# Kernel tuning notes

Measured on AMD Instinct MI355X. Metric: run time of the kernel, lower is better.

Reference implementation:

```python
import jax, jax.numpy as jnp
import numpy as np

GAMMA = 0.99
LMBDA = 0.95


def setup_inputs() -> dict:
    key = jax.random.key(0)
    k1, k2, k3, k4 = jax.random.split(key, 4)
    B, T = 8192, 2048
    reward = jax.random.normal(k1, (B, T), dtype=jnp.float32)
    terminated = jax.random.randint(k2, (B, T), 0, 2).astype(jnp.bool_)
    value = jax.random.normal(k3, (B, T), dtype=jnp.float32)
    next_value = jax.random.normal(k4, (B, T), dtype=jnp.float32)
    return {"reward": reward, "terminated": terminated, "value": value, "next_value": next_value}


def reference(reward, terminated, value, next_value):
    # not_done: [B, T]
    not_done = 1.0 - terminated.astype(reward.dtype)
    # fake_bootstrap=False branch: zero out next_value at terminal steps
    delta = reward + GAMMA * (next_value * not_done) - value  # [B, T]
    coef = (GAMMA * LMBDA) * not_done                          # [B, T]

    def step(gae, xs):
        d_t, c_t = xs                 # each [B]
        gae = d_t + c_t * gae
        return gae, gae

    init = jnp.zeros(reward.shape[0], dtype=reward.dtype)
    # scan backward in time over [T, B] slices; reverse=True keeps outputs
    # aligned with the original time indices.
    _, adv_t = jax.lax.scan(step, init, (delta.T, coef.T), reverse=True)
    advantages = adv_t.T              # [B, T]
    returns = advantages + value
    return advantages, returns
```

## Files before the change

### kernel.cpp

```cpp
#include <hip/hip_runtime.h>


#define GAMMA 0.99f
#define LMBDA 0.95f

constexpr int T_LEN      = 2048;
constexpr int PER_THREAD = 4;
constexpr int BLOCK      = T_LEN / PER_THREAD;
constexpr int NWAVE      = BLOCK / 64;

__global__ __launch_bounds__(BLOCK) void gae_kernel(
    const float* __restrict__ reward,
    const int*   __restrict__ terminated,
    const float* __restrict__ value,
    const float* __restrict__ next_value,
    float* __restrict__ adv_out,
    float* __restrict__ ret_out)
{
    const int b   = blockIdx.x;
    const int j   = threadIdx.x;
    const size_t base = (size_t)b * T_LEN + (size_t)j * PER_THREAD;

    float4 r0 = *(const float4*)(reward     + base);
    float4 v0 = *(const float4*)(value      + base);
    float4 n0 = *(const float4*)(next_value + base);
    int4   tA = *(const int4*)  (terminated + base);

    float rr[4] = {r0.x, r0.y, r0.z, r0.w};
    float vv[4] = {v0.x, v0.y, v0.z, v0.w};
    float nn[4] = {n0.x, n0.y, n0.z, n0.w};
    int   tt[4] = {tA.x, tA.y, tA.z, tA.w};

    float delta[4], coef[4];
#pragma unroll
    for (int i = 0; i < 4; ++i) {
        float nd = tt[i] ? 0.0f : 1.0f;
        delta[i] = rr[i] + GAMMA * nn[i] * nd - vv[i];
        coef[i]  = (GAMMA * LMBDA) * nd;
    }

    float A = 0.0f, P = 1.0f;
#pragma unroll
    for (int i = 3; i >= 0; --i) {
        A = delta[i] + coef[i] * A;
        P = coef[i] * P;
    }

    const int lane = j & 63;
    const int wave = j >> 6;
    float SA = A, SP = P;
#pragma unroll
    for (int o = 1; o < 64; o <<= 1) {
        float A2 = __shfl_down(SA, o, 64);
        float P2 = __shfl_down(SP, o, 64);
        if (lane + o < 64) {
            SA = SA + SP * A2;
            SP = SP * P2;
        }
    }
    float EA = __shfl_down(SA, 1, 64);
    float EP = __shfl_down(SP, 1, 64);
    if (lane == 63) { EA = 0.0f; EP = 1.0f; }

    __shared__ float wA[NWAVE];
    __shared__ float wP[NWAVE];
    if (lane == 0) { wA[wave] = SA; wP[wave] = SP; }
    __syncthreads();

    float accA = 0.0f;
    for (int ww = NWAVE - 1; ww > wave; --ww) {
        accA = wA[ww] + wP[ww] * accA;
    }

    float g = EA + EP * accA;

    float adv[4];
#pragma unroll
    for (int i = 3; i >= 0; --i) {
        g = delta[i] + coef[i] * g;
        adv[i] = g;
    }

    float4 a0 = {adv[0], adv[1], adv[2], adv[3]};
    float4 q0 = {adv[0] + vv[0], adv[1] + vv[1], adv[2] + vv[2], adv[3] + vv[3]};

    *(float4*)(adv_out + base) = a0;
    *(float4*)(ret_out + base) = q0;
}

extern "C" void kernel_launch(void* const* d_in, const int* in_sizes, int n_in,
                              void* d_out, int out_size, void* d_ws, size_t ws_size,
                              hipStream_t stream) {
    const float* reward     = (const float*)d_in[0];
    const int*   terminated = (const int*)  d_in[1];
    const float* value      = (const float*)d_in[2];
    const float* next_value = (const float*)d_in[3];

    const int total = in_sizes[0];
    const int B     = total / T_LEN;

    float* adv = (float*)d_out;
    float* ret = (float*)d_out + (size_t)total;

    gae_kernel<<<B, BLOCK, 0, stream>>>(reward, terminated, value, next_value, adv, ret);
}
```

Measured before the change: 317.0 us.

## Process each row with a single wave over eight segments, dropping LDS sync

Replaces the 512-thread block per row, which needed a cross-wave shared-memory combine and __syncthreads, with one 64-lane wave per row. Each lane handles 8 segments of 4 elements, and the segment carries are combined through wave shuffles plus a short serial chain over lane-0 values. This removes the block barrier and LDS traffic and gives more independent shuffle chains to interleave. In exchange it uses many more registers per thread (about 32 loaded floats per input array), which may lower occupancy in a memory-bound kernel, and each wave has more serial work.

Result: no change. 321.8 us (+1.5%).

```diff
diff --git a/kernel.cpp b/kernel.cpp
--- a/kernel.cpp
+++ b/kernel.cpp
@@ -4,12 +4,11 @@
 #define GAMMA 0.99f
 #define LMBDA 0.95f
 
-constexpr int T_LEN      = 2048;
-constexpr int PER_THREAD = 4;
-constexpr int BLOCK      = T_LEN / PER_THREAD;
-constexpr int NWAVE      = BLOCK / 64;
+constexpr int T_LEN  = 2048;
+constexpr int SEGS   = 8;
+constexpr int SEGLEN = 256;
 
-__global__ __launch_bounds__(BLOCK) void gae_kernel(
+__global__ __launch_bounds__(64) void gae_kernel(
     const float* __restrict__ reward,
     const int*   __restrict__ terminated,
     const float* __restrict__ value,
@@ -17,75 +16,94 @@
     float* __restrict__ adv_out,
     float* __restrict__ ret_out)
 {
-    const int b   = blockIdx.x;
-    const int j   = threadIdx.x;
-    const size_t base = (size_t)b * T_LEN + (size_t)j * PER_THREAD;
+    const int b    = blockIdx.x;
+    const int lane = threadIdx.x;
+    const size_t rowbase = (size_t)b * T_LEN;
 
-    float4 r0 = *(const float4*)(reward     + base);
-    float4 v0 = *(const float4*)(value      + base);
-    float4 n0 = *(const float4*)(next_value + base);
-    int4   tA = *(const int4*)  (terminated + base);
-
-    float rr[4] = {r0.x, r0.y, r0.z, r0.w};
-    float vv[4] = {v0.x, v0.y, v0.z, v0.w};
-    float nn[4] = {n0.x, n0.y, n0.z, n0.w};
-    int   tt[4] = {tA.x, tA.y, tA.z, tA.w};
-
-    float delta[4], coef[4];
+    float4 R[SEGS], V[SEGS], N[SEGS];
+    int4   Tm[SEGS];
 #pragma unroll
-    for (int i = 0; i < 4; ++i) {
-        float nd = tt[i] ? 0.0f : 1.0f;
-        delta[i] = rr[i] + GAMMA * nn[i] * nd - vv[i];
-        coef[i]  = (GAMMA * LMBDA) * nd;
+    for (int i = 0; i < SEGS; ++i) {
+        const size_t off = rowbase + (size_t)i * SEGLEN + (size_t)lane * 4;
+        R[i]  = *(const float4*)(reward     + off);
+        V[i]  = *(const float4*)(value      + off);
+        N[i]  = *(const float4*)(next_value + off);
+        Tm[i] = *(const int4*)  (terminated + off);
     }
 
-    float A = 0.0f, P = 1.0f;
+    float delta[SEGS][4], coef[SEGS][4], vv[SEGS][4];
 #pragma unroll
-    for (int i = 3; i >= 0; --i) {
-        A = delta[i] + coef[i] * A;
-        P = coef[i] * P;
+    for (int i = 0; i < SEGS; ++i) {
+        float rr[4] = {R[i].x, R[i].y, R[i].z, R[i].w};
+        float nn[4] = {N[i].x, N[i].y, N[i].z, N[i].w};
+        int   tt[4] = {Tm[i].x, Tm[i].y, Tm[i].z, Tm[i].w};
+        vv[i][0] = V[i].x; vv[i][1] = V[i].y; vv[i][2] = V[i].z; vv[i][3] = V[i].w;
+#pragma unroll
+        for (int k = 0; k < 4; ++k) {
+            float nd = tt[k] ? 0.0f : 1.0f;
+            delta[i][k] = rr[k] + GAMMA * nn[k] * nd - vv[i][k];
+            coef[i][k]  = (GAMMA * LMBDA) * nd;
+        }
     }
 
-    const int lane = j & 63;
-    const int wave = j >> 6;
-    float SA = A, SP = P;
+    float SA[SEGS], SP[SEGS];
+#pragma unroll
+    for (int i = 0; i < SEGS; ++i) {
+        float A = 0.0f, P = 1.0f;
+#pragma unroll
+        for (int k = 3; k >= 0; --k) {
+            A = delta[i][k] + coef[i][k] * A;
+            P = coef[i][k] * P;
+        }
+        SA[i] = A; SP[i] = P;
+    }
+
 #pragma unroll
     for (int o = 1; o < 64; o <<= 1) {
-        float A2 = __shfl_down(SA, o, 64);
-        float P2 = __shfl_down(SP, o, 64);
-        if (lane + o < 64) {
-            SA = SA + SP * A2;
-            SP = SP * P2;
+#pragma unroll
+        for (int i = 0; i < SEGS; ++i) {
+            float A2 = __shfl_down(SA[i], o, 64);
+            float P2 = __shfl_down(SP[i], o, 64);
+            if (lane + o < 64) {
+                SA[i] = SA[i] + SP[i] * A2;
+                SP[i] = SP[i] * P2;
+            }
         }
     }
-    float EA = __shfl_down(SA, 1, 64);
-    float EP = __shfl_down(SP, 1, 64);
-    if (lane == 63) { EA = 0.0f; EP = 1.0f; }
-
-    __shared__ float wA[NWAVE];
-    __shared__ float wP[NWAVE];
-    if (lane == 0) { wA[wave] = SA; wP[wave] = SP; }
-    __syncthreads();
-
-    float accA = 0.0f;
-    for (int ww = NWAVE - 1; ww > wave; --ww) {
-        accA = wA[ww] + wP[ww] * accA;
+    float EA[SEGS], EP[SEGS];
+#pragma unroll
+    for (int i = 0; i < SEGS; ++i) {
+        EA[i] = __shfl_down(SA[i], 1, 64);
+        EP[i] = __shfl_down(SP[i], 1, 64);
+        if (lane == 63) { EA[i] = 0.0f; EP[i] = 1.0f; }
     }
 
-    float g = EA + EP * accA;
-
-    float adv[4];
+    float xin[SEGS];
+    float acc = 0.0f;
 #pragma unroll
-    for (int i = 3; i >= 0; --i) {
-        g = delta[i] + coef[i] * g;
-        adv[i] = g;
+    for (int i = SEGS - 1; i >= 0; --i) {
+        xin[i] = acc;
+        float Ga = __shfl(SA[i], 0, 64);
+        float Gp = __shfl(SP[i], 0, 64);
+        acc = Ga + Gp * acc;
     }
 
-    float4 a0 = {adv[0], adv[1], adv[2], adv[3]};
-    float4 q0 = {adv[0] + vv[0], adv[1] + vv[1], adv[2] + vv[2], adv[3] + vv[3]};
-
-    *(float4*)(adv_out + base) = a0;
-    *(float4*)(ret_out + base) = q0;
+#pragma unroll
+    for (int i = 0; i < SEGS; ++i) {
+        float g = EA[i] + EP[i] * xin[i];
+        float adv[4];
+#pragma unroll
+        for (int k = 3; k >= 0; --k) {
+            g = delta[i][k] + coef[i][k] * g;
+            adv[k] = g;
+        }
+        float4 a0 = {adv[0], adv[1], adv[2], adv[3]};
+        float4 q0 = {adv[0] + vv[i][0], adv[1] + vv[i][1],
+                     adv[2] + vv[i][2], adv[3] + vv[i][3]};
+        const size_t off = rowbase + (size_t)i * SEGLEN + (size_t)lane * 4;
+        *(float4*)(adv_out + off) = a0;
+        *(float4*)(ret_out + off) = q0;
+    }
 }
 
 extern "C" void kernel_launch(void* const* d_in, const int* in_sizes, int n_in,
@@ -102,5 +120,5 @@
     float* adv = (float*)d_out;
     float* ret = (float*)d_out + (size_t)total;
 
-    gae_kernel<<<B, BLOCK, 0, stream>>>(reward, terminated, value, next_value, adv, ret);
+    gae_kernel<<<B, 64, 0, stream>>>(reward, terminated, value, next_value, adv, ret);
 }
```
